# Kernel tuning notes

Hardware: AMD Instinct MI355X
Metric: run time of the kernel (lower is better)

The kernel has to match this reference:

```python
import jax, jax.numpy as jnp
import numpy as np

B, IN, D, H, S = 128, 1024, 128, 512, 256  # batch, in_dim, out_dim, mlp hidden, gibbs samples


def _bern_logprob(v, logits):
    # sum_i v_i*logit_i - softplus(logit_i)  (Bernoulli log-likelihood)
    return jnp.sum(v * logits - jax.nn.softplus(logits), axis=-1)


def _energy_f(zv, wv, W1, b1, W2, b2):
    # unnormalized log p(w|z): MLP on concat(z, w) -> scalar per sample
    pre = zv @ W1[:, :D].T + wv @ W1[:, D:].T + b1  # [..., H]
    return (jax.nn.relu(pre) @ W2.T + b2)[..., 0]


def setup_inputs() -> dict:
    key = jax.random.key(0)
    ks = jax.random.split(key, 10)
    x = jax.random.bernoulli(ks[0], 0.5, (B, IN)).astype(jnp.float32)
    y = jax.random.bernoulli(ks[1], 0.5, (B, IN)).astype(jnp.float32)
    W = 0.02 * jax.random.normal(ks[2], (IN, D), dtype=jnp.float32)
    b = 0.02 * jax.random.normal(ks[3], (D,), dtype=jnp.float32)
    c = 0.02 * jax.random.normal(ks[4], (IN,), dtype=jnp.float32)
    W1 = jax.random.normal(ks[5], (H, 2 * D), dtype=jnp.float32) / np.sqrt(2.0 * D)
    b1 = jnp.zeros((H,), dtype=jnp.float32)
    W2 = jax.random.normal(ks[6], (1, H), dtype=jnp.float32) / np.sqrt(float(H))
    b2 = jnp.zeros((1,), dtype=jnp.float32)
    # encoder_sample_: w ~ Bernoulli(sigmoid(x @ W + b)) (detached in original)
    w = jax.random.bernoulli(ks[7], jax.nn.sigmoid(x @ W + b)).astype(jnp.float32)
    z = jax.random.bernoulli(ks[8], jax.nn.sigmoid(y @ W + b)).astype(jnp.float32)
    # Gibbs chain output (detached); uniform-binary stand-in for the 4-sweep sampler
    w_tilde = jax.random.bernoulli(ks[9], 0.5, (S, B, D)).astype(jnp.float32)
    return {"x": x, "y": y, "w": w, "z": z, "w_tilde": w_tilde,
            "W": W, "b": b, "c": c, "W1": W1, "b1": b1, "W2": W2, "b2": b2}


def reference(x, y, w, z, w_tilde, W, b, c, W1, b1, W2, b2):
    # log p(x|w): decoder logits = w W^T + c
    log_pxw = _bern_logprob(x, w @ W.T + c)          # [B]
    # log p(w|x): encoder logits = x W + b
    log_pwx = _bern_logprob(w, x @ W + b)            # [B]
    # estimated normalized log p(w|z) under the EBM (MC estimate of log Z)
    f_zw = _energy_f(z, w, W1, b1, W2, b2)           # [B]
    f_tilde = _energy_f(z[None], w_tilde, W1, b1, W2, b2)  # [S,B]
    logZ = jax.nn.logsumexpr if False else (jax.nn.logsumexp(f_tilde, axis=0) - jnp.log(jnp.float32(S)) + jnp.float32(D) * jnp.log(jnp.float32(2.0)))
    r_wz = jnp.minimum(f_zw - logZ, 0.0)             # [B]
    # NegativeMILoss returns -(p_x_w - p_w_x + r_w_z)
    return -(log_pxw - log_pwx + r_wz)
```

## Files before the change

### kernel.cpp

```cpp
#include <hip/hip_runtime.h>
#include <hip/hip_bf16.h>
#include <math.h>

#define B_ 128
#define IN_ 1024
#define D_ 128
#define H_ 512
#define S_ 256

typedef __attribute__((ext_vector_type(8))) short short8v;
typedef __attribute__((ext_vector_type(8))) unsigned short ushort8v;
typedef __attribute__((ext_vector_type(4))) unsigned short ushort4v;
typedef __attribute__((ext_vector_type(4))) float f32x4;

__device__ __forceinline__ float softplusf(float x) {
  return fmaxf(x, 0.f) + log1pf(expf(-fabsf(x)));
}

__device__ __forceinline__ unsigned short f2bf(float f) {
  unsigned u = __float_as_uint(f);
  unsigned r = (u + 0x7fff + ((u >> 16) & 1)) >> 16;
  return (unsigned short)r;
}

__device__ __forceinline__ short8v ld_frag8(const float* __restrict__ p) {
  const float4 v0 = *(const float4*)(p);
  const float4 v1 = *(const float4*)(p + 4);
  short8v s;
  s[0] = (short)f2bf(v0.x); s[1] = (short)f2bf(v0.y);
  s[2] = (short)f2bf(v0.z); s[3] = (short)f2bf(v0.w);
  s[4] = (short)f2bf(v1.x); s[5] = (short)f2bf(v1.y);
  s[6] = (short)f2bf(v1.z); s[7] = (short)f2bf(v1.w);
  return s;
}

__global__ __launch_bounds__(256) void Kpack(
    const float* __restrict__ x, const float* __restrict__ W,
    const float* __restrict__ W1,
    unsigned short* __restrict__ Bp, unsigned short* __restrict__ Bz,
    unsigned short* __restrict__ BwT, float* __restrict__ l2part) {
  __shared__ float smem[512];
  const int blk = blockIdx.x;
  const int t = threadIdx.x;

  if (blk < 128) {
    const int zhalf = (blk >= 64);
    const int o = ((blk & 63) * 256 + t) * 4;
    const int frag = o >> 9;
    const int l = (o >> 3) & 63;
    const int j0 = o & 7;
    const int h = (frag >> 2) * 16 + (l & 15);
    const int k0 = (frag & 3) * 32 + ((l >> 4) << 3) + j0;
    const float4 v = *(const float4*)(W1 + (size_t)h * 256 + (zhalf ? 0 : 128) + k0);
    ushort4v u;
    u[0] = f2bf(v.x); u[1] = f2bf(v.y); u[2] = f2bf(v.z); u[3] = f2bf(v.w);
    *(ushort4v*)((zhalf ? Bz : Bp) + o) = u;
  } else if (blk < 256) {
    const int o = ((blk - 128) * 256 + t) * 4;
    const int frag = o >> 9;
    const int l = (o >> 3) & 63;
    const int j0 = o & 7;
    const int i = (frag >> 2) * 16 + (l & 15);
    const int k0 = (frag & 3) * 32 + ((l >> 4) << 3) + j0;
    const float4 v = *(const float4*)(W + (size_t)i * D_ + k0);
    ushort4v u;
    u[0] = f2bf(v.x); u[1] = f2bf(v.y); u[2] = f2bf(v.z); u[3] = f2bf(v.w);
    *(ushort4v*)(BwT + o) = u;
  } else {
    const int bb = blk - 256;
    const int b = bb >> 3, kc = bb & 7;
    float* xs = smem;
    float* p2 = smem + 128;
    if (t < 128) xs[t] = x[b * IN_ + kc * 128 + t];
    __syncthreads();
    const int d = t & 127, ks = t >> 7;
    const float* __restrict__ Wp = W + (size_t)(kc * 128 + ks * 64) * D_ + d;
    float s = 0.f;
    #pragma unroll 8
    for (int i = 0; i < 64; ++i) s = fmaf(xs[ks * 64 + i], Wp[(size_t)i * D_], s);
    p2[ks * 128 + d] = s;
    __syncthreads();
    if (t < 128) l2part[((size_t)b * 8 + kc) * 128 + t] = p2[t] + p2[128 + t];
  }
}

__global__ __launch_bounds__(256) void Kmm(
    const float* __restrict__ w, const float* __restrict__ z,
    const float* __restrict__ x, const float* __restrict__ cvec,
    const float* __restrict__ b1, const float* __restrict__ W2,
    const unsigned short* __restrict__ Bp, const unsigned short* __restrict__ Bz,
    const unsigned short* __restrict__ BwT, float* __restrict__ zb1,
    float* __restrict__ pxw_part, float* __restrict__ fzw_part) {
  __shared__ float xs[16][128];
  __shared__ float redp[4][16];
  const int blk = blockIdx.x;
  const int t = threadIdx.x;
  const int lane = t & 63, wv = t >> 6;

  if (blk < 64) {
    const int bt = blk >> 3, ic = blk & 7;
    {
      const int row = t >> 4, c8 = (t & 15) * 8;
      const float* __restrict__ src = x + (size_t)(bt * 16 + row) * IN_ + ic * 128 + c8;
      *(float4*)&xs[row][c8]     = *(const float4*)(src);
      *(float4*)&xs[row][c8 + 4] = *(const float4*)(src + 4);
    }
    short8v a[4];
    const int arow = bt * 16 + (lane & 15);
    const int k0 = (lane >> 4) * 8;
    #pragma unroll
    for (int ks = 0; ks < 4; ++ks)
      a[ks] = ld_frag8(w + (size_t)arow * D_ + ks * 32 + k0);
    __syncthreads();

    float term[4] = {0.f, 0.f, 0.f, 0.f};
    #pragma unroll
    for (int itl = 0; itl < 2; ++itl) {
      const int itile = wv * 2 + itl;
      const int git = ic * 8 + itile;
      f32x4 acc = {0.f, 0.f, 0.f, 0.f};
      #pragma unroll
      for (int ks = 0; ks < 4; ++ks) {
        const short8v bfr = *(const short8v*)(BwT + ((size_t)(git * 4 + ks) << 9) + (lane << 3));
        acc = __builtin_amdgcn_mfma_f32_16x16x32_bf16(a[ks], bfr, acc, 0, 0, 0);
      }
      const int iloc = itile * 16 + (lane & 15);
      const float cv = cvec[ic * 128 + iloc];
      #pragma unroll
      for (int j = 0; j < 4; ++j) {
        const int rloc = (lane >> 4) * 4 + j;
        const float lg = acc[j] + cv;
        term[j] += xs[rloc][iloc] * lg - softplusf(lg);
      }
    }
    #pragma unroll
    for (int j = 0; j < 4; ++j) {
      float v = term[j];
      v += __shfl_xor(v, 1); v += __shfl_xor(v, 2);
      v += __shfl_xor(v, 4); v += __shfl_xor(v, 8);
      if ((lane & 15) == 0) redp[wv][(lane >> 4) * 4 + j] = v;
    }
    __syncthreads();
    if (t < 16)
      pxw_part[(size_t)(bt * 16 + t) * 8 + ic] =
          redp[0][t] + redp[1][t] + redp[2][t] + redp[3][t];
  } else {
    const int bb = blk - 64;
    const int bt = bb >> 2, hc = bb & 3;
    short8v az[4], aw[4];
    const int arow = bt * 16 + (lane & 15);
    const int k0 = (lane >> 4) * 8;
    #pragma unroll
    for (int ks = 0; ks < 4; ++ks) {
      az[ks] = ld_frag8(z + (size_t)arow * D_ + ks * 32 + k0);
      aw[ks] = ld_frag8(w + (size_t)arow * D_ + ks * 32 + k0);
    }
    float term[4] = {0.f, 0.f, 0.f, 0.f};
    #pragma unroll
    for (int htl = 0; htl < 2; ++htl) {
      const int ghb = hc * 8 + wv * 2 + htl;
      f32x4 accz = {0.f, 0.f, 0.f, 0.f};
      f32x4 accw = {0.f, 0.f, 0.f, 0.f};
      #pragma unroll
      for (int ks = 0; ks < 4; ++ks) {
        const size_t fo = ((size_t)(ghb * 4 + ks) << 9) + (lane << 3);
        const short8v bz = *(const short8v*)(Bz + fo);
        const short8v bw = *(const short8v*)(Bp + fo);
        accz = __builtin_amdgcn_mfma_f32_16x16x32_bf16(az[ks], bz, accz, 0, 0, 0);
        accw = __builtin_amdgcn_mfma_f32_16x16x32_bf16(aw[ks], bw, accw, 0, 0, 0);
      }
      const int h = ghb * 16 + (lane & 15);
      const float b1v = b1[h], w2v = W2[h];
      #pragma unroll
      for (int j = 0; j < 4; ++j) {
        const int brow = bt * 16 + (lane >> 4) * 4 + j;
        const float zp = accz[j] + b1v;
        zb1[(size_t)brow * H_ + h] = zp;
        term[j] += fmaxf(zp + accw[j], 0.f) * w2v;
      }
    }
    #pragma unroll
    for (int j = 0; j < 4; ++j) {
      float v = term[j];
      v += __shfl_xor(v, 1); v += __shfl_xor(v, 2);
      v += __shfl_xor(v, 4); v += __shfl_xor(v, 8);
      if ((lane & 15) == 0) redp[wv][(lane >> 4) * 4 + j] = v;
    }
    __syncthreads();
    if (t < 16)
      fzw_part[(size_t)(bt * 16 + t) * 4 + hc] =
          redp[0][t] + redp[1][t] + redp[2][t] + redp[3][t];
  }
}

__global__ __launch_bounds__(1024) void Kmain(
    const float* __restrict__ wt, const unsigned short* __restrict__ Bp,
    const float* __restrict__ zb1, const float* __restrict__ W2,
    const float* __restrict__ b2, const float* __restrict__ l2part,
    const float* __restrict__ bvec, const float* __restrict__ w,
    const float* __restrict__ pxw_part, const float* __restrict__ fzw_part,
    float* __restrict__ out) {
  const int b = blockIdx.x;
  const int t = threadIdx.x;
  const int lane = t & 63, wvid = t >> 6;
  const int sc = wvid >> 2, nh = (wvid >> 1) & 1, nth = wvid & 1;

  __shared__ unsigned short atile[256 * 128];
  __shared__ float zb1s[H_];
  __shared__ float w2s[H_];
  __shared__ float red[16][64];
  __shared__ float mred[4], ered[4], pred[2], miscs[2];

  if (t < 512) { zb1s[t] = zb1[(size_t)b * H_ + t]; w2s[t] = W2[t]; }

  {
    const int r = t >> 2;
    const int g0 = (t & 3) * 4;
    const float* __restrict__ src = wt + ((size_t)r * B_ + b) * D_;
    #pragma unroll
    for (int gg = 0; gg < 4; ++gg) {
      const int g = g0 + gg;
      const float4 v0 = *(const float4*)(src + g * 8);
      const float4 v1 = *(const float4*)(src + g * 8 + 4);
      ushort8v u;
      u[0] = f2bf(v0.x); u[1] = f2bf(v0.y); u[2] = f2bf(v0.z); u[3] = f2bf(v0.w);
      u[4] = f2bf(v1.x); u[5] = f2bf(v1.y); u[6] = f2bf(v1.z); u[7] = f2bf(v1.w);
      *(ushort8v*)&atile[r * 128 + ((g ^ (r & 15)) << 3)] = u;
    }
  }
  __syncthreads();

  short8v afr[4][4];
  #pragma unroll
  for (int m = 0; m < 4; ++m) {
    const int arow = sc * 64 + m * 16 + (lane & 15);
    #pragma unroll
    for (int ks = 0; ks < 4; ++ks) {
      const int g = ks * 4 + (lane >> 4);
      afr[m][ks] = *(const short8v*)&atile[arow * 128 + ((g ^ (arow & 15)) << 3)];
    }
  }

  float fsum[4][4];
  #pragma unroll
  for (int m = 0; m < 4; ++m)
    #pragma unroll
    for (int j = 0; j < 4; ++j) fsum[m][j] = 0.f;

  const int hl = lane & 15;
  #pragma unroll 2
  for (int nt = 0; nt < 8; ++nt) {
    const int hblk = nh * 16 + nth * 8 + nt;
    const int hrow = hblk * 16 + hl;
    f32x4 acc0 = {0.f,0.f,0.f,0.f}, acc1 = {0.f,0.f,0.f,0.f};
    f32x4 acc2 = {0.f,0.f,0.f,0.f}, acc3 = {0.f,0.f,0.f,0.f};
    #pragma unroll
    for (int ks = 0; ks < 4; ++ks) {
      const int frag = hblk * 4 + ks;
      const short8v bfr = *(const short8v*)(Bp + ((size_t)frag << 9) + (lane << 3));
      acc0 = __builtin_amdgcn_mfma_f32_16x16x32_bf16(afr[0][ks], bfr, acc0, 0, 0, 0);
      acc1 = __builtin_amdgcn_mfma_f32_16x16x32_bf16(afr[1][ks], bfr, acc1, 0, 0, 0);
      acc2 = __builtin_amdgcn_mfma_f32_16x16x32_bf16(afr[2][ks], bfr, acc2, 0, 0, 0);
      acc3 = __builtin_amdgcn_mfma_f32_16x16x32_bf16(afr[3][ks], bfr, acc3, 0, 0, 0);
    }
    const float zv = zb1s[hrow], wgt = w2s[hrow];
    #pragma unroll
    for (int j = 0; j < 4; ++j) {
      fsum[0][j] += fmaxf(acc0[j] + zv, 0.f) * wgt;
      fsum[1][j] += fmaxf(acc1[j] + zv, 0.f) * wgt;
      fsum[2][j] += fmaxf(acc2[j] + zv, 0.f) * wgt;
      fsum[3][j] += fmaxf(acc3[j] + zv, 0.f) * wgt;
    }
  }
  #pragma unroll
  for (int m = 0; m < 4; ++m)
    #pragma unroll
    for (int j = 0; j < 4; ++j) {
      float v = fsum[m][j];
      v += __shfl_xor(v, 1); v += __shfl_xor(v, 2);
      v += __shfl_xor(v, 4); v += __shfl_xor(v, 8);
      fsum[m][j] = v;
    }
  if (hl == 0) {
    const int rb = (lane >> 4) * 4;
    #pragma unroll
    for (int m = 0; m < 4; ++m)
      #pragma unroll
      for (int j = 0; j < 4; ++j)
        red[wvid][m * 16 + rb + j] = fsum[m][j];
  }
  __syncthreads();

  float fval = 0.f;
  if (t < 256) {
    const int sc2 = t >> 6, r = t & 63;
    fval = red[sc2 * 4 + 0][r] + red[sc2 * 4 + 1][r]
         + red[sc2 * 4 + 2][r] + red[sc2 * 4 + 3][r] + b2[0];
    float mm = fval;
    #pragma unroll
    for (int o = 1; o < 64; o <<= 1) mm = fmaxf(mm, __shfl_xor(mm, o));
    if (lane == 0) mred[wvid] = mm;
  } else if (t < 384) {
    const int d = t - 256;
    float lg = bvec[d];
    #pragma unroll
    for (int kc = 0; kc < 8; ++kc) lg += l2part[((size_t)b * 8 + kc) * 128 + d];
    float term = w[b * 128 + d] * lg - softplusf(lg);
    #pragma unroll
    for (int o = 1; o < 64; o <<= 1) term += __shfl_xor(term, o);
    if (lane == 0) pred[wvid - 4] = term;
  } else if (t == 384) {
    float s = 0.f;
    #pragma unroll
    for (int ic = 0; ic < 8; ++ic) s += pxw_part[(size_t)b * 8 + ic];
    miscs[0] = s;
  } else if (t == 385) {
    float s = 0.f;
    #pragma unroll
    for (int hc = 0; hc < 4; ++hc) s += fzw_part[(size_t)b * 4 + hc];
    miscs[1] = s;
  }
  __syncthreads();
  if (t < 256) {
    const float mm = fmaxf(fmaxf(mred[0], mred[1]), fmaxf(mred[2], mred[3]));
    float e = expf(fval - mm);
    #pragma unroll
    for (int o = 1; o < 64; o <<= 1) e += __shfl_xor(e, o);
    if (lane == 0) ered[wvid] = e;
  }
  __syncthreads();
  if (t == 0) {
    const float mm = fmaxf(fmaxf(mred[0], mred[1]), fmaxf(mred[2], mred[3]));
    const float tot = ered[0] + ered[1] + ered[2] + ered[3];
    const float logZ = mm + logf(tot) - logf((float)S_) + (float)D_ * logf(2.f);
    const float pwx = pred[0] + pred[1];
    const float pxw = miscs[0];
    const float fzw = miscs[1] + b2[0];
    const float r_wz = fminf(fzw - logZ, 0.f);
    out[b] = -(pxw - pwx + r_wz);
  }
}

extern "C" void kernel_launch(void* const* d_in, const int* in_sizes, int n_in,
                              void* d_out, int out_size, void* d_ws, size_t ws_size,
                              hipStream_t stream) {
  const float* x    = (const float*)d_in[0];
  const float* w    = (const float*)d_in[2];
  const float* z    = (const float*)d_in[3];
  const float* wt   = (const float*)d_in[4];
  const float* W    = (const float*)d_in[5];
  const float* bvec = (const float*)d_in[6];
  const float* cvec = (const float*)d_in[7];
  const float* W1   = (const float*)d_in[8];
  const float* b1   = (const float*)d_in[9];
  const float* W2   = (const float*)d_in[10];
  const float* b2   = (const float*)d_in[11];

  float* ws_f = (float*)d_ws;
  unsigned short* Bp    = (unsigned short*)ws_f;
  unsigned short* Bz    = (unsigned short*)(ws_f + 32768);
  unsigned short* BwT   = (unsigned short*)(ws_f + 65536);
  float* zb1            = ws_f + 131072;
  float* l2part         = ws_f + 196608;
  float* pxw_part       = ws_f + 327680;
  float* fzw_part       = ws_f + 328704;
  float* out = (float*)d_out;

  hipLaunchKernelGGL(Kpack, dim3(1280), dim3(256), 0, stream,
                     x, W, W1, Bp, Bz, BwT, l2part);
  hipLaunchKernelGGL(Kmm, dim3(96), dim3(256), 0, stream,
                     w, z, x, cvec, b1, W2, Bp, Bz, BwT, zb1, pxw_part, fzw_part);
  hipLaunchKernelGGL(Kmain, dim3(B_), dim3(1024), 0, stream,
                     wt, Bp, zb1, W2, b2, l2part, bvec, w, pxw_part, fzw_part, out);
}
```

Measured before the change: 32.23 us.

## Compute encoder logits x@W with bf16 MFMA in Kmm2 instead of scalar Kpack blocks

```diff
diff --git a/kernel.cpp b/kernel.cpp
--- a/kernel.cpp
+++ b/kernel.cpp
@@ -34,12 +34,10 @@
   return s;
 }
 
-__global__ __launch_bounds__(256) void Kpack(
-    const float* __restrict__ x, const float* __restrict__ W,
-    const float* __restrict__ W1,
+__global__ __launch_bounds__(256) void Kpack2(
+    const float* __restrict__ W, const float* __restrict__ W1,
     unsigned short* __restrict__ Bp, unsigned short* __restrict__ Bz,
-    unsigned short* __restrict__ BwT, float* __restrict__ l2part) {
-  __shared__ float smem[512];
+    unsigned short* __restrict__ BwT, unsigned short* __restrict__ BdT) {
   const int blk = blockIdx.x;
   const int t = threadIdx.x;
 
@@ -67,32 +65,41 @@
     u[0] = f2bf(v.x); u[1] = f2bf(v.y); u[2] = f2bf(v.z); u[3] = f2bf(v.w);
     *(ushort4v*)(BwT + o) = u;
   } else {
-    const int bb = blk - 256;
-    const int b = bb >> 3, kc = bb & 7;
-    float* xs = smem;
-    float* p2 = smem + 128;
-    if (t < 128) xs[t] = x[b * IN_ + kc * 128 + t];
-    __syncthreads();
-    const int d = t & 127, ks = t >> 7;
-    const float* __restrict__ Wp = W + (size_t)(kc * 128 + ks * 64) * D_ + d;
-    float s = 0.f;
-    #pragma unroll 8
-    for (int i = 0; i < 64; ++i) s = fmaf(xs[ks * 64 + i], Wp[(size_t)i * D_], s);
-    p2[ks * 128 + d] = s;
-    __syncthreads();
-    if (t < 128) l2part[((size_t)b * 8 + kc) * 128 + t] = p2[t] + p2[128 + t];
-  }
-}
-
-__global__ __launch_bounds__(256) void Kmm(
+    const int o = ((blk - 256) * 256 + t) * 4;
+    const int frag = o >> 9;
+    const int l = (o >> 3) & 63;
+    const int j0 = o & 7;
+    const int d = (frag >> 5) * 16 + (l & 15);
+    const int k0 = (frag & 31) * 32 + ((l >> 4) << 3) + j0;
+    ushort4v u;
+    u[0] = f2bf(W[(size_t)(k0 + 0) * D_ + d]);
+    u[1] = f2bf(W[(size_t)(k0 + 1) * D_ + d]);
+    u[2] = f2bf(W[(size_t)(k0 + 2) * D_ + d]);
+    u[3] = f2bf(W[(size_t)(k0 + 3) * D_ + d]);
+    *(ushort4v*)(BdT + o) = u;
+  }
+}
+
+union SMemM {
+  struct { float xs[16][128]; float redp[4][16]; } px;
+  struct { float redp[4][16]; } zw;
+  struct {
+    unsigned short xtile[16 * 1024];
+    float redk[4][2][16][16];
+    float tsum[16][32];
+  } pw;
+};
+
+__global__ __launch_bounds__(256) void Kmm2(
     const float* __restrict__ w, const float* __restrict__ z,
     const float* __restrict__ x, const float* __restrict__ cvec,
-    const float* __restrict__ b1, const float* __restrict__ W2,
+    const float* __restrict__ bvec, const float* __restrict__ b1,
+    const float* __restrict__ W2,
     const unsigned short* __restrict__ Bp, const unsigned short* __restrict__ Bz,
-    const unsigned short* __restrict__ BwT, float* __restrict__ zb1,
-    float* __restrict__ pxw_part, float* __restrict__ fzw_part) {
-  __shared__ float xs[16][128];
-  __shared__ float redp[4][16];
+    const unsigned short* __restrict__ BwT, const unsigned short* __restrict__ BdT,
+    float* __restrict__ zb1, float* __restrict__ pxw_part,
+    float* __restrict__ fzw_part, float* __restrict__ pwx_part) {
+  __shared__ SMemM sm;
   const int blk = blockIdx.x;
   const int t = threadIdx.x;
   const int lane = t & 63, wv = t >> 6;
@@ -102,8 +109,8 @@
     {
       const int row = t >> 4, c8 = (t & 15) * 8;
       const float* __restrict__ src = x + (size_t)(bt * 16 + row) * IN_ + ic * 128 + c8;
-      *(float4*)&xs[row][c8]     = *(const float4*)(src);
-      *(float4*)&xs[row][c8 + 4] = *(const float4*)(src + 4);
+      *(float4*)&sm.px.xs[row][c8]     = *(const float4*)(src);
+      *(float4*)&sm.px.xs[row][c8 + 4] = *(const float4*)(src + 4);
     }
     short8v a[4];
     const int arow = bt * 16 + (lane & 15);
@@ -130,7 +137,7 @@
       for (int j = 0; j < 4; ++j) {
         const int rloc = (lane >> 4) * 4 + j;
         const float lg = acc[j] + cv;
-        term[j] += xs[rloc][iloc] * lg - softplusf(lg);
+        term[j] += sm.px.xs[rloc][iloc] * lg - softplusf(lg);
       }
     }
     #pragma unroll
@@ -138,13 +145,13 @@
       float v = term[j];
       v += __shfl_xor(v, 1); v += __shfl_xor(v, 2);
       v += __shfl_xor(v, 4); v += __shfl_xor(v, 8);
-      if ((lane & 15) == 0) redp[wv][(lane >> 4) * 4 + j] = v;
+      if ((lane & 15) == 0) sm.px.redp[wv][(lane >> 4) * 4 + j] = v;
     }
     __syncthreads();
     if (t < 16)
       pxw_part[(size_t)(bt * 16 + t) * 8 + ic] =
-          redp[0][t] + redp[1][t] + redp[2][t] + redp[3][t];
-  } else {
+          sm.px.redp[0][t] + sm.px.redp[1][t] + sm.px.redp[2][t] + sm.px.redp[3][t];
+  } else if (blk < 96) {
     const int bb = blk - 64;
     const int bt = bb >> 2, hc = bb & 3;
     short8v az[4], aw[4];
@@ -184,21 +191,78 @@
       float v = term[j];
       v += __shfl_xor(v, 1); v += __shfl_xor(v, 2);
       v += __shfl_xor(v, 4); v += __shfl_xor(v, 8);
-      if ((lane & 15) == 0) redp[wv][(lane >> 4) * 4 + j] = v;
+      if ((lane & 15) == 0) sm.zw.redp[wv][(lane >> 4) * 4 + j] = v;
     }
     __syncthreads();
     if (t < 16)
       fzw_part[(size_t)(bt * 16 + t) * 4 + hc] =
-          redp[0][t] + redp[1][t] + redp[2][t] + redp[3][t];
+          sm.zw.redp[0][t] + sm.zw.redp[1][t] + sm.zw.redp[2][t] + sm.zw.redp[3][t];
+  } else {
+    const int bb = blk - 96;
+    const int bt = bb >> 2, dp = bb & 3;
+    {
+      const int r = t >> 4;
+      const int gbase = (t & 15) * 8;
+      const float* __restrict__ src = x + (size_t)(bt * 16 + r) * IN_;
+      #pragma unroll
+      for (int gg = 0; gg < 8; ++gg) {
+        const int g = gbase + gg;
+        const float4 v0 = *(const float4*)(src + g * 8);
+        const float4 v1 = *(const float4*)(src + g * 8 + 4);
+        ushort8v u;
+        u[0] = f2bf(v0.x); u[1] = f2bf(v0.y); u[2] = f2bf(v0.z); u[3] = f2bf(v0.w);
+        u[4] = f2bf(v1.x); u[5] = f2bf(v1.y); u[6] = f2bf(v1.z); u[7] = f2bf(v1.w);
+        const int gs = (g & ~15) | ((g & 15) ^ (r & 15));
+        *(ushort8v*)&sm.pw.xtile[r * 1024 + gs * 8] = u;
+      }
+    }
+    __syncthreads();
+
+    f32x4 acc0 = {0.f, 0.f, 0.f, 0.f}, acc1 = {0.f, 0.f, 0.f, 0.f};
+    const int r = lane & 15;
+    #pragma unroll
+    for (int kk = 0; kk < 8; ++kk) {
+      const int ks = wv * 8 + kk;
+      const int g = ks * 4 + (lane >> 4);
+      const int gs = (g & ~15) | ((g & 15) ^ r);
+      const short8v a = *(const short8v*)&sm.pw.xtile[r * 1024 + gs * 8];
+      const short8v b0 = *(const short8v*)(BdT + ((size_t)((dp * 2 + 0) * 32 + ks) << 9) + (lane << 3));
+      const short8v b1f = *(const short8v*)(BdT + ((size_t)((dp * 2 + 1) * 32 + ks) << 9) + (lane << 3));
+      acc0 = __builtin_amdgcn_mfma_f32_16x16x32_bf16(a, b0, acc0, 0, 0, 0);
+      acc1 = __builtin_amdgcn_mfma_f32_16x16x32_bf16(a, b1f, acc1, 0, 0, 0);
+    }
+    #pragma unroll
+    for (int j = 0; j < 4; ++j) {
+      sm.pw.redk[wv][0][(lane >> 4) * 4 + j][lane & 15] = acc0[j];
+      sm.pw.redk[wv][1][(lane >> 4) * 4 + j][lane & 15] = acc1[j];
+    }
+    __syncthreads();
+    #pragma unroll
+    for (int ee = 0; ee < 2; ++ee) {
+      const int e = t + ee * 256;
+      const int dt = e >> 8, row = (e >> 4) & 15, col = e & 15;
+      const int d = (dp * 2 + dt) * 16 + col;
+      const int bglob = bt * 16 + row;
+      const float lg = sm.pw.redk[0][dt][row][col] + sm.pw.redk[1][dt][row][col]
+                     + sm.pw.redk[2][dt][row][col] + sm.pw.redk[3][dt][row][col]
+                     + bvec[d];
+      sm.pw.tsum[row][dt * 16 + col] = w[(size_t)bglob * D_ + d] * lg - softplusf(lg);
+    }
+    __syncthreads();
+    if (t < 16) {
+      float s = 0.f;
+      #pragma unroll
+      for (int dd = 0; dd < 32; ++dd) s += sm.pw.tsum[t][dd];
+      pwx_part[(size_t)(bt * 16 + t) * 4 + dp] = s;
+    }
   }
 }
 
 __global__ __launch_bounds__(1024) void Kmain(
     const float* __restrict__ wt, const unsigned short* __restrict__ Bp,
     const float* __restrict__ zb1, const float* __restrict__ W2,
-    const float* __restrict__ b2, const float* __restrict__ l2part,
-    const float* __restrict__ bvec, const float* __restrict__ w,
-    const float* __restrict__ pxw_part, const float* __restrict__ fzw_part,
+    const float* __restrict__ b2, const float* __restrict__ pxw_part,
+    const float* __restrict__ fzw_part, const float* __restrict__ pwx_part,
     float* __restrict__ out) {
   const int b = blockIdx.x;
   const int t = threadIdx.x;
@@ -209,7 +273,7 @@
   __shared__ float zb1s[H_];
   __shared__ float w2s[H_];
   __shared__ float red[16][64];
-  __shared__ float mred[4], ered[4], pred[2], miscs[2];
+  __shared__ float mred[4], ered[4], miscs[3];
 
   if (t < 512) { zb1s[t] = zb1[(size_t)b * H_ + t]; w2s[t] = W2[t]; }
 
@@ -300,25 +364,21 @@
     #pragma unroll
     for (int o = 1; o < 64; o <<= 1) mm = fmaxf(mm, __shfl_xor(mm, o));
     if (lane == 0) mred[wvid] = mm;
-  } else if (t < 384) {
-    const int d = t - 256;
-    float lg = bvec[d];
-    #pragma unroll
-    for (int kc = 0; kc < 8; ++kc) lg += l2part[((size_t)b * 8 + kc) * 128 + d];
-    float term = w[b * 128 + d] * lg - softplusf(lg);
-    #pragma unroll
-    for (int o = 1; o < 64; o <<= 1) term += __shfl_xor(term, o);
-    if (lane == 0) pred[wvid - 4] = term;
-  } else if (t == 384) {
+  } else if (t == 256) {
     float s = 0.f;
     #pragma unroll
     for (int ic = 0; ic < 8; ++ic) s += pxw_part[(size_t)b * 8 + ic];
     miscs[0] = s;
-  } else if (t == 385) {
+  } else if (t == 257) {
     float s = 0.f;
     #pragma unroll
     for (int hc = 0; hc < 4; ++hc) s += fzw_part[(size_t)b * 4 + hc];
     miscs[1] = s;
+  } else if (t == 258) {
+    float s = 0.f;
+    #pragma unroll
+    for (int dp = 0; dp < 4; ++dp) s += pwx_part[(size_t)b * 4 + dp];
+    miscs[2] = s;
   }
   __syncthreads();
   if (t < 256) {
@@ -333,9 +393,9 @@
     const float mm = fmaxf(fmaxf(mred[0], mred[1]), fmaxf(mred[2], mred[3]));
     const float tot = ered[0] + ered[1] + ered[2] + ered[3];
     const float logZ = mm + logf(tot) - logf((float)S_) + (float)D_ * logf(2.f);
-    const float pwx = pred[0] + pred[1];
     const float pxw = miscs[0];
     const float fzw = miscs[1] + b2[0];
+    const float pwx = miscs[2];
     const float r_wz = fminf(fzw - logZ, 0.f);
     out[b] = -(pxw - pwx + r_wz);
   }
@@ -360,16 +420,18 @@
   unsigned short* Bp    = (unsigned short*)ws_f;
   unsigned short* Bz    = (unsigned short*)(ws_f + 32768);
   unsigned short* BwT   = (unsigned short*)(ws_f + 65536);
-  float* zb1            = ws_f + 131072;
-  float* l2part         = ws_f + 196608;
-  float* pxw_part       = ws_f + 327680;
-  float* fzw_part       = ws_f + 328704;
+  unsigned short* BdT   = (unsigned short*)(ws_f + 131072);
+  float* zb1            = ws_f + 196608;
+  float* pxw_part       = ws_f + 262144;
+  float* fzw_part       = ws_f + 263168;
+  float* pwx_part       = ws_f + 263680;
   float* out = (float*)d_out;
 
-  hipLaunchKernelGGL(Kpack, dim3(1280), dim3(256), 0, stream,
-                     x, W, W1, Bp, Bz, BwT, l2part);
-  hipLaunchKernelGGL(Kmm, dim3(96), dim3(256), 0, stream,
-                     w, z, x, cvec, b1, W2, Bp, Bz, BwT, zb1, pxw_part, fzw_part);
+  hipLaunchKernelGGL(Kpack2, dim3(384), dim3(256), 0, stream,
+                     W, W1, Bp, Bz, BwT, BdT);
+  hipLaunchKernelGGL(Kmm2, dim3(128), dim3(256), 0, stream,
+                     w, z, x, cvec, bvec, b1, W2, Bp, Bz, BwT, BdT,
+                     zb1, pxw_part, fzw_part, pwx_part);
   hipLaunchKernelGGL(Kmain, dim3(B_), dim3(1024), 0, stream,
-                     wt, Bp, zb1, W2, b2, l2part, bvec, w, pxw_part, fzw_part, out);
-}
+                     wt, Bp, zb1, W2, b2, pxw_part, fzw_part, pwx_part, out);
+}
```

New measurement: 33.91 us. 5.2% more time.
